# Kernel optimization log

Measured on AMD Instinct MI355X. Metric: run time of the kernel, lower is better.

## Reference

```python
import jax, jax.numpy as jnp
import numpy as np

N_NODES = 100000
N_EDGES = 3200000
IN_DIM = 64
N_SEQ = 8
HID1 = 256
HID2 = 128
END = 64
OUT = 1


def _glorot(key, shape):
    fan_in, fan_out = shape
    lim = (6.0 / (fan_in + fan_out)) ** 0.5
    return jax.random.uniform(key, shape, jnp.float32, -lim, lim)


def setup_inputs() -> dict:
    key = jax.random.key(0)
    ks = jax.random.split(key, 10)
    features = jax.random.normal(ks[0], (N_NODES, IN_DIM, N_SEQ), jnp.float32)
    src = jax.random.randint(ks[1], (N_EDGES,), 0, N_NODES, jnp.int32)
    dst = jax.random.randint(ks[2], (N_EDGES,), 0, N_NODES, jnp.int32)
    return {
        "features": features,
        "src": src,
        "dst": dst,
        "W1": _glorot(ks[3], (IN_DIM * N_SEQ, HID1)),
        "b1": jnp.zeros((HID1,), jnp.float32),
        "W2": _glorot(ks[4], (HID1, HID2)),
        "b2": jnp.zeros((HID2,), jnp.float32),
        "Wo1": _glorot(ks[5], (HID2, END)),
        "bo1": jnp.zeros((END,), jnp.float32),
        "Wo2": _glorot(ks[6], (END, OUT)),
        "bo2": jnp.zeros((OUT,), jnp.float32),
    }


def _graph_conv(x, src, dst, W, b):
    # DGL GraphConv, norm='both': D_out^{-1/2} pre-scale, sum-aggregate, D_in^{-1/2} post-scale.
    n = x.shape[0]
    ones = jnp.ones((src.shape[0],), x.dtype)
    deg_out = jnp.clip(jax.ops.segment_sum(ones, src, num_segments=n), 1.0)
    deg_in = jnp.clip(jax.ops.segment_sum(ones, dst, num_segments=n), 1.0)
    x = x * jax.lax.rsqrt(deg_out)[:, None]
    # mult-first vs aggregate-first is mathematically identical; project to smaller dim first
    if W.shape[0] > W.shape[1]:
        x = x @ W
        agg = jax.ops.segment_sum(x[src], dst, num_segments=n)
    else:
        agg = jax.ops.segment_sum(x[src], dst, num_segments=n) @ W
    return agg * jax.lax.rsqrt(deg_in)[:, None] + b


def reference(features, src, dst, W1, b1, W2, b2, Wo1, bo1, Wo2, bo2):
    x = features.reshape(features.shape[0], IN_DIM * N_SEQ)  # [N, in_dim*n_seq]
    x = jax.nn.relu(_graph_conv(x, src, dst, W1, b1))
    x = _graph_conv(x, src, dst, W2, b2)
    x = jax.nn.relu(x @ Wo1 + bo1)
    return x @ Wo2 + bo2
```

## Files before the change

### kernel.cpp

```cpp
#include <hip/hip_runtime.h>
#include <hip/hip_bf16.h>
#include <hip/hip_fp16.h>

#define N_NODES 100000
#define N_EDGES 3200000
#define DIM0 512
#define DIM1 256
#define DIM2 128
#define DIM3 64
#define NSB 98

#define HPART 16384
#define HPAIR 8192
#define NP 7
#define NSL 32
#define SLC (N_EDGES / NSL)

typedef _Float16 f16x8 __attribute__((ext_vector_type(8)));
typedef float f32x4 __attribute__((ext_vector_type(4)));


__global__ __launch_bounds__(256) void k_hist_priv(const int* __restrict__ src,
                                                   const int* __restrict__ dst,
                                                   unsigned* __restrict__ hp) {
    __shared__ unsigned h32[HPAIR];
    int blk = blockIdx.x, part = blockIdx.y, arr = blockIdx.z;
    const int* __restrict__ keys = arr ? dst : src;
    int base = part * HPART;
    for (int i = threadIdx.x; i < HPAIR; i += 256) h32[i] = 0;
    __syncthreads();
    int e0 = blk * SLC, e1 = e0 + SLC;
    for (int e = e0 + threadIdx.x; e < e1; e += 256) {
        int k = keys[e] - base;
        if ((unsigned)k < (unsigned)HPART)
            atomicAdd(&h32[k >> 1], 1u << ((k & 1) * 16));
    }
    __syncthreads();
    unsigned* out = hp + ((size_t)(arr * NP + part) * NSL + blk) * HPAIR;
    for (int i = threadIdx.x; i < HPAIR; i += 256) out[i] = h32[i];
}

__global__ __launch_bounds__(256) void k_reduce(unsigned* __restrict__ hp,
                                                int* __restrict__ cnt_out,
                                                int* __restrict__ cnt_in) {
    int idx = blockIdx.x * 256 + threadIdx.x;
    if (idx >= 2 * NP * HPAIR) return;
    int arr = idx / (NP * HPAIR);
    int rem = idx % (NP * HPAIR);
    int part = rem / HPAIR;
    int j = rem % HPAIR;
    unsigned* p = hp + ((size_t)(arr * NP + part) * NSL) * HPAIR + j;
    unsigned lo = 0, hi = 0;
    #pragma unroll 8
    for (int b = 0; b < NSL; ++b) {
        unsigned v = p[(size_t)b * HPAIR];
        if (arr == 1) p[(size_t)b * HPAIR] = (lo & 0xffffu) | (hi << 16);
        lo += v & 0xffffu;
        hi += v >> 16;
    }
    int node0 = part * HPART + 2 * j;
    int* cnt = arr ? cnt_in : cnt_out;
    if (node0 < N_NODES) cnt[node0] = (int)lo;
    if (node0 + 1 < N_NODES) cnt[node0 + 1] = (int)hi;
}

__global__ __launch_bounds__(1024) void k_scan_a(const int* __restrict__ cnt,
                                                 int* __restrict__ excl,
                                                 int* __restrict__ bsum) {
    __shared__ int buf[1024];
    int tid = threadIdx.x;
    int i = blockIdx.x * 1024 + tid;
    int v = (i < N_NODES) ? cnt[i] : 0;
    buf[tid] = v;
    __syncthreads();
    #pragma unroll
    for (int off = 1; off < 1024; off <<= 1) {
        int t = (tid >= off) ? buf[tid - off] : 0;
        __syncthreads();
        buf[tid] += t;
        __syncthreads();
    }
    if (i < N_NODES) excl[i] = buf[tid] - v;
    if (tid == 1023) bsum[blockIdx.x] = buf[1023];
}

__global__ __launch_bounds__(128) void k_scan_b(const int* __restrict__ bsum,
                                                int* __restrict__ boff) {
    __shared__ int buf[128];
    int tid = threadIdx.x;
    int v = (tid < NSB) ? bsum[tid] : 0;
    buf[tid] = v;
    __syncthreads();
    #pragma unroll
    for (int off = 1; off < 128; off <<= 1) {
        int t = (tid >= off) ? buf[tid - off] : 0;
        __syncthreads();
        buf[tid] += t;
        __syncthreads();
    }
    if (tid < NSB) boff[tid] = buf[tid] - v;
    if (tid == 127) boff[NSB] = buf[127];
}

__global__ __launch_bounds__(256) void k_scan_c(const int* __restrict__ excl,
                                                const int* __restrict__ boff,
                                                const int* __restrict__ cnt_out,
                                                const int* __restrict__ cnt_in,
                                                int* __restrict__ row_ptr,
                                                float* __restrict__ s_out,
                                                float* __restrict__ s_in) {
    int i = blockIdx.x * 256 + threadIdx.x;
    if (i < N_NODES) {
        row_ptr[i] = excl[i] + boff[i >> 10];
        int co = cnt_out[i]; if (co < 1) co = 1;
        int ci = cnt_in[i];  if (ci < 1) ci = 1;
        s_out[i] = rsqrtf((float)co);
        s_in[i]  = rsqrtf((float)ci);
    }
    if (i == 0) row_ptr[N_NODES] = boff[NSB];
}

__global__ __launch_bounds__(256) void k_scatter_nr(const int* __restrict__ src,
                                                    const int* __restrict__ dst,
                                                    const int* __restrict__ row_ptr,
                                                    const unsigned* __restrict__ hp,
                                                    int* __restrict__ esrc) {
    __shared__ int base_s[HPART];
    int blk = blockIdx.x, part = blockIdx.y;
    int pbase = part * HPART;
    const unsigned* off_p = hp + ((size_t)(1 * NP + part) * NSL + blk) * HPAIR;
    for (int k = threadIdx.x; k < HPART; k += 256) {
        int node = pbase + k;
        int rp = (node < N_NODES) ? row_ptr[node] : 0;
        unsigned w = off_p[k >> 1];
        unsigned off = (k & 1) ? (w >> 16) : (w & 0xffffu);
        base_s[k] = rp + (int)off;
    }
    __syncthreads();
    int e0 = blk * SLC, e1 = e0 + SLC;
    for (int e = e0 + threadIdx.x; e < e1; e += 256) {
        int d = dst[e];
        int k = d - pbase;
        if ((unsigned)k < (unsigned)HPART) {
            int p = atomicAdd(&base_s[k], 1);
            esrc[p] = src[e];
        }
    }
}


__global__ __launch_bounds__(256) void k_cvtW1(const float* __restrict__ W1,
                                               __half* __restrict__ W1t) {
    int idx = blockIdx.x * 256 + threadIdx.x;
    if (idx < DIM0 * DIM1) {
        int k = idx / DIM1, n = idx % DIM1;
        W1t[n * DIM0 + k] = __float2half(W1[idx]);
    }
}

__global__ __launch_bounds__(256) void k_cvtW2(const float* __restrict__ W2,
                                               __half* __restrict__ W2t) {
    int idx = blockIdx.x * 256 + threadIdx.x;
    if (idx < DIM1 * DIM2) {
        int k = idx / DIM2, n = idx % DIM2;
        W2t[n * DIM1 + k] = __float2half(W2[idx]);
    }
}


__global__ __launch_bounds__(256) void k_gemm1(const float* __restrict__ feat,
                                               const float* __restrict__ s_out,
                                               const __half* __restrict__ W1t,
                                               __half* __restrict__ y) {
    __shared__ __align__(16) _Float16 As[64][40];
    __shared__ __align__(16) _Float16 Bs[256][40];
    int tid = threadIdx.x;
    int wv = tid >> 6, lane = tid & 63;
    int m16 = lane & 15, quad = lane >> 4;
    int n0 = blockIdx.x * 64;

    int srow = tid >> 2;
    int scol = (tid & 3) * 8;
    int gr = n0 + srow;
    bool avalid = gr < N_NODES;
    int grc = avalid ? gr : (N_NODES - 1);
    float ascale = avalid ? s_out[gr] : 0.0f;
    const float* aptr = feat + (size_t)grc * DIM0 + scol;
    int bn = tid >> 2;
    int bc = (tid & 3) * 8;

    f32x4 acc[4][4] = {};
    for (int k0 = 0; k0 < DIM0; k0 += 32) {
        float4 f0 = *(const float4*)(aptr + k0);
        float4 f1 = *(const float4*)(aptr + k0 + 4);
        __syncthreads();
        {
            f16x8 h;
            h[0] = (_Float16)(f0.x * ascale); h[1] = (_Float16)(f0.y * ascale);
            h[2] = (_Float16)(f0.z * ascale); h[3] = (_Float16)(f0.w * ascale);
            h[4] = (_Float16)(f1.x * ascale); h[5] = (_Float16)(f1.y * ascale);
            h[6] = (_Float16)(f1.z * ascale); h[7] = (_Float16)(f1.w * ascale);
            *(f16x8*)&As[srow][scol] = h;
        }
        #pragma unroll
        for (int p = 0; p < 4; ++p) {
            int n = p * 64 + bn;
            f16x8 v = *(const f16x8*)(W1t + (size_t)n * DIM0 + k0 + bc);
            *(f16x8*)&Bs[n][bc] = v;
        }
        __syncthreads();
        f16x8 af[4], bf[4];
        #pragma unroll
        for (int r = 0; r < 4; ++r) af[r] = *(const f16x8*)&As[r * 16 + m16][quad * 8];
        #pragma unroll
        for (int c = 0; c < 4; ++c) bf[c] = *(const f16x8*)&Bs[wv * 64 + c * 16 + m16][quad * 8];
        #pragma unroll
        for (int r = 0; r < 4; ++r)
            #pragma unroll
            for (int c = 0; c < 4; ++c)
                acc[r][c] = __builtin_amdgcn_mfma_f32_16x16x32_f16(af[r], bf[c], acc[r][c], 0, 0, 0);
    }
    #pragma unroll
    for (int r = 0; r < 4; ++r) {
        #pragma unroll
        for (int i = 0; i < 4; ++i) {
            int row = n0 + r * 16 + quad * 4 + i;
            if (row < N_NODES) {
                #pragma unroll
                for (int c = 0; c < 4; ++c) {
                    int col = wv * 64 + c * 16 + m16;
                    y[(size_t)row * DIM1 + col] = __float2half(acc[r][c][i]);
                }
            }
        }
    }
}


__global__ __launch_bounds__(256) void k_agg256(const int* __restrict__ row_ptr,
                                                const int* __restrict__ esrc,
                                                const __half* __restrict__ y1,
                                                const float* __restrict__ s_in,
                                                const float* __restrict__ s_out,
                                                const float* __restrict__ b1,
                                                __half* __restrict__ x2) {
    int wave = threadIdx.x >> 6;
    int lane = threadIdx.x & 63;
    int n = blockIdx.x * 4 + wave;
    int beg = row_ptr[n], end = row_ptr[n + 1];
    const uint2* ybase = (const uint2*)y1;
    float4 acc = make_float4(0.f, 0.f, 0.f, 0.f);
    int i = beg;
    for (; i + 4 <= end; i += 4) {
        int s0 = esrc[i], s1 = esrc[i + 1], s2 = esrc[i + 2], s3 = esrc[i + 3];
        uint2 r0 = ybase[(size_t)s0 * 64 + lane];
        uint2 r1 = ybase[(size_t)s1 * 64 + lane];
        uint2 r2 = ybase[(size_t)s2 * 64 + lane];
        uint2 r3 = ybase[(size_t)s3 * 64 + lane];
        float2 a0 = __half22float2(*(__half2*)&r0.x), b0 = __half22float2(*(__half2*)&r0.y);
        float2 a1 = __half22float2(*(__half2*)&r1.x), b1v = __half22float2(*(__half2*)&r1.y);
        float2 a2 = __half22float2(*(__half2*)&r2.x), b2v = __half22float2(*(__half2*)&r2.y);
        float2 a3 = __half22float2(*(__half2*)&r3.x), b3v = __half22float2(*(__half2*)&r3.y);
        acc.x += a0.x + a1.x + a2.x + a3.x;
        acc.y += a0.y + a1.y + a2.y + a3.y;
        acc.z += b0.x + b1v.x + b2v.x + b3v.x;
        acc.w += b0.y + b1v.y + b2v.y + b3v.y;
    }
    for (; i < end; ++i) {
        uint2 r = ybase[(size_t)esrc[i] * 64 + lane];
        float2 a = __half22float2(*(__half2*)&r.x), b = __half22float2(*(__half2*)&r.y);
        acc.x += a.x; acc.y += a.y; acc.z += b.x; acc.w += b.y;
    }
    float si = s_in[n];
    float so = s_out[n];
    float4 bb = *(const float4*)&b1[lane * 4];
    acc.x = fmaxf(acc.x * si + bb.x, 0.f) * so;
    acc.y = fmaxf(acc.y * si + bb.y, 0.f) * so;
    acc.z = fmaxf(acc.z * si + bb.z, 0.f) * so;
    acc.w = fmaxf(acc.w * si + bb.w, 0.f) * so;
    union { uint2 u; __half2 h[2]; } cv;
    cv.h[0] = __floats2half2_rn(acc.x, acc.y);
    cv.h[1] = __floats2half2_rn(acc.z, acc.w);
    *(uint2*)&x2[(size_t)n * DIM1 + lane * 4] = cv.u;
}


__global__ __launch_bounds__(256) void k_gemm2(const __half* __restrict__ x2,
                                               const __half* __restrict__ W2t,
                                               __half* __restrict__ y) {
    __shared__ __align__(16) _Float16 As[64][40];
    __shared__ __align__(16) _Float16 Bs[128][40];
    int tid = threadIdx.x;
    int wv = tid >> 6, lane = tid & 63;
    int m16 = lane & 15, quad = lane >> 4;
    int n0 = blockIdx.x * 64;

    int srow = tid >> 2;
    int scol = (tid & 3) * 8;
    int gr = n0 + srow;
    int grc = (gr < N_NODES) ? gr : (N_NODES - 1);
    const __half* aptr = x2 + (size_t)grc * DIM1 + scol;
    int bn = tid >> 2;
    int bc = (tid & 3) * 8;

    f32x4 acc[4][2] = {};
    for (int k0 = 0; k0 < DIM1; k0 += 32) {
        f16x8 av = *(const f16x8*)(aptr + k0);
        __syncthreads();
        *(f16x8*)&As[srow][scol] = av;
        #pragma unroll
        for (int p = 0; p < 2; ++p) {
            int n = p * 64 + bn;
            f16x8 v = *(const f16x8*)(W2t + (size_t)n * DIM1 + k0 + bc);
            *(f16x8*)&Bs[n][bc] = v;
        }
        __syncthreads();
        f16x8 af[4], bf[2];
        #pragma unroll
        for (int r = 0; r < 4; ++r) af[r] = *(const f16x8*)&As[r * 16 + m16][quad * 8];
        #pragma unroll
        for (int c = 0; c < 2; ++c) bf[c] = *(const f16x8*)&Bs[wv * 32 + c * 16 + m16][quad * 8];
        #pragma unroll
        for (int r = 0; r < 4; ++r)
            #pragma unroll
            for (int c = 0; c < 2; ++c)
                acc[r][c] = __builtin_amdgcn_mfma_f32_16x16x32_f16(af[r], bf[c], acc[r][c], 0, 0, 0);
    }
    #pragma unroll
    for (int r = 0; r < 4; ++r) {
        #pragma unroll
        for (int i = 0; i < 4; ++i) {
            int row = n0 + r * 16 + quad * 4 + i;
            if (row < N_NODES) {
                #pragma unroll
                for (int c = 0; c < 2; ++c) {
                    int col = wv * 32 + c * 16 + m16;
                    y[(size_t)row * DIM2 + col] = __float2half(acc[r][c][i]);
                }
            }
        }
    }
}


__global__ __launch_bounds__(256) void k_agg_head(const int* __restrict__ row_ptr,
                                                  const int* __restrict__ esrc,
                                                  const __half* __restrict__ y2,
                                                  const float* __restrict__ s_in,
                                                  const float* __restrict__ b2,
                                                  const float* __restrict__ Wo1,
                                                  const float* __restrict__ bo1,
                                                  const float* __restrict__ Wo2,
                                                  const float* __restrict__ bo2,
                                                  float* __restrict__ out) {
    __shared__ __half2 w1p[DIM2 / 2][DIM3];
    __shared__ float w2s[DIM3];
    __shared__ float hs[4][DIM2];
    int tid = threadIdx.x;
    for (int i = tid; i < (DIM2 / 2) * DIM3; i += 256) {
        int m = i >> 6, l = i & 63;
        w1p[m][l] = __floats2half2_rn(Wo1[(2 * m) * DIM3 + l], Wo1[(2 * m + 1) * DIM3 + l]);
    }
    if (tid < DIM3) w2s[tid] = Wo2[tid];
    __syncthreads();

    int wave = tid >> 6, lane = tid & 63;
    int n = blockIdx.x * 4 + wave;
    int beg = row_ptr[n], end = row_ptr[n + 1];
    const unsigned* ybase = (const unsigned*)y2;
    float2 acc = make_float2(0.f, 0.f);
    int i = beg;
    for (; i + 4 <= end; i += 4) {
        unsigned r0 = ybase[(size_t)esrc[i] * 64 + lane];
        unsigned r1 = ybase[(size_t)esrc[i + 1] * 64 + lane];
        unsigned r2 = ybase[(size_t)esrc[i + 2] * 64 + lane];
        unsigned r3 = ybase[(size_t)esrc[i + 3] * 64 + lane];
        float2 f0 = __half22float2(*(__half2*)&r0);
        float2 f1 = __half22float2(*(__half2*)&r1);
        float2 f2 = __half22float2(*(__half2*)&r2);
        float2 f3 = __half22float2(*(__half2*)&r3);
        acc.x += f0.x + f1.x + f2.x + f3.x;
        acc.y += f0.y + f1.y + f2.y + f3.y;
    }
    for (; i < end; ++i) {
        unsigned r = ybase[(size_t)esrc[i] * 64 + lane];
        float2 f = __half22float2(*(__half2*)&r);
        acc.x += f.x; acc.y += f.y;
    }
    float si = s_in[n];
    float2 bv = *(const float2*)&b2[lane * 2];
    hs[wave][lane * 2 + 0] = acc.x * si + bv.x;
    hs[wave][lane * 2 + 1] = acc.y * si + bv.y;
    __syncthreads();

    float t = bo1[lane];
    #pragma unroll 8
    for (int m = 0; m < DIM2 / 2; ++m) {
        float2 h2 = *(const float2*)&hs[wave][2 * m];
        float2 wf = __half22float2(w1p[m][lane]);
        t += h2.x * wf.x + h2.y * wf.y;
    }
    t = fmaxf(t, 0.f);
    float p = t * w2s[lane];
    #pragma unroll
    for (int off = 32; off > 0; off >>= 1) p += __shfl_down(p, off);
    if (lane == 0) out[n] = p + bo2[0];
}


extern "C" void kernel_launch(void* const* d_in, const int* in_sizes, int n_in,
                              void* d_out, int out_size, void* d_ws, size_t ws_size,
                              hipStream_t stream) {
    const float* feat = (const float*)d_in[0];
    const int*   src  = (const int*)d_in[1];
    const int*   dst  = (const int*)d_in[2];
    const float* W1   = (const float*)d_in[3];
    const float* b1   = (const float*)d_in[4];
    const float* W2   = (const float*)d_in[5];
    const float* b2   = (const float*)d_in[6];
    const float* Wo1  = (const float*)d_in[7];
    const float* bo1  = (const float*)d_in[8];
    const float* Wo2  = (const float*)d_in[9];
    const float* bo2  = (const float*)d_in[10];
    float* out = (float*)d_out;

    char* ws = (char*)d_ws;
    size_t off = 0;
    auto alloc = [&](size_t bytes) -> char* {
        char* p = ws + off;
        off = (off + bytes + 255) & ~(size_t)255;
        return p;
    };
    int*      cnt_out = (int*)alloc(N_NODES * 4);
    int*      cnt_in  = (int*)alloc(N_NODES * 4);
    int*      row_ptr = (int*)alloc((N_NODES + 1) * 4);
    int*      excl    = (int*)alloc(N_NODES * 4);
    int*      bsum    = (int*)alloc((NSB + 1) * 4);
    int*      boff    = (int*)alloc((NSB + 1) * 4);
    int*      esrc    = (int*)alloc((size_t)N_EDGES * 4);
    unsigned* histp   = (unsigned*)alloc((size_t)2 * NP * NSL * HPAIR * 4);
    float*    s_out   = (float*)alloc(N_NODES * 4);
    float*    s_in    = (float*)alloc(N_NODES * 4);
    __half*   W1t     = (__half*)alloc((size_t)DIM0 * DIM1 * 2);
    __half*   W2t     = (__half*)alloc((size_t)DIM1 * DIM2 * 2);
    __half*   y1h     = (__half*)alloc((size_t)N_NODES * DIM1 * 2);
    __half*   x2h     = (__half*)alloc((size_t)N_NODES * DIM1 * 2);
    __half*   y2h     = (__half*)alloc((size_t)N_NODES * DIM2 * 2);

    k_hist_priv<<<dim3(NSL, NP, 2), 256, 0, stream>>>(src, dst, histp);
    k_reduce<<<(2 * NP * HPAIR + 255) / 256, 256, 0, stream>>>(histp, cnt_out, cnt_in);
    k_scan_a<<<NSB, 1024, 0, stream>>>(cnt_in, excl, bsum);
    k_scan_b<<<1, 128, 0, stream>>>(bsum, boff);
    k_scan_c<<<(N_NODES + 255) / 256, 256, 0, stream>>>(excl, boff, cnt_out, cnt_in,
                                                        row_ptr, s_out, s_in);
    k_scatter_nr<<<dim3(NSL, NP), 256, 0, stream>>>(src, dst, row_ptr, histp, esrc);

    k_cvtW1<<<(DIM0 * DIM1 + 255) / 256, 256, 0, stream>>>(W1, W1t);
    k_cvtW2<<<(DIM1 * DIM2 + 255) / 256, 256, 0, stream>>>(W2, W2t);

    int nblk = (N_NODES + 63) / 64;
    k_gemm1<<<nblk, 256, 0, stream>>>(feat, s_out, W1t, y1h);
    k_agg256<<<N_NODES / 4, 256, 0, stream>>>(row_ptr, esrc, y1h, s_in, s_out, b1, x2h);
    k_gemm2<<<nblk, 256, 0, stream>>>(x2h, W2t, y2h);
    k_agg_head<<<N_NODES / 4, 256, 0, stream>>>(row_ptr, esrc, y2h, s_in, b2,
                                                Wo1, bo1, Wo2, bo2, out);
}
```

Before: 1.166 ms.

## Widen aggregation gathers to 16B loads and split head into MFMA kernel

Both aggregation kernels now gather each neighbor row with 16-byte loads per lane. A wave processes 2 or 4 edges at once in subgroups and combines the partial sums with cross-lane shuffles. The fused aggregate+MLP head is split into a pure aggregation kernel that writes an fp16 intermediate, plus a separate MFMA-based head kernel that uses a pre-transposed fp16 Wo1. The goal is more bytes in flight per gather and removing the per-block shared-memory weight staging and scalar dot loop in the head. The cost is an extra intermediate buffer, an extra launch, and fp16 rounding of the head input.

```diff
diff --git a/kernel.cpp b/kernel.cpp
--- a/kernel.cpp
+++ b/kernel.cpp
@@ -149,21 +149,24 @@
 }
 
 
-__global__ __launch_bounds__(256) void k_cvtW1(const float* __restrict__ W1,
-                                               __half* __restrict__ W1t) {
+__global__ __launch_bounds__(256) void k_cvtW(const float* __restrict__ W1,
+                                              const float* __restrict__ W2,
+                                              const float* __restrict__ Wo1,
+                                              __half* __restrict__ W1t,
+                                              __half* __restrict__ W2t,
+                                              __half* __restrict__ Wo1t) {
     int idx = blockIdx.x * 256 + threadIdx.x;
     if (idx < DIM0 * DIM1) {
         int k = idx / DIM1, n = idx % DIM1;
         W1t[n * DIM0 + k] = __float2half(W1[idx]);
-    }
-}
-
-__global__ __launch_bounds__(256) void k_cvtW2(const float* __restrict__ W2,
-                                               __half* __restrict__ W2t) {
-    int idx = blockIdx.x * 256 + threadIdx.x;
-    if (idx < DIM1 * DIM2) {
-        int k = idx / DIM2, n = idx % DIM2;
-        W2t[n * DIM1 + k] = __float2half(W2[idx]);
+    } else if (idx < DIM0 * DIM1 + DIM1 * DIM2) {
+        int j = idx - DIM0 * DIM1;
+        int k = j / DIM2, n = j % DIM2;
+        W2t[n * DIM1 + k] = __float2half(W2[j]);
+    } else if (idx < DIM0 * DIM1 + DIM1 * DIM2 + DIM2 * DIM3) {
+        int j = idx - DIM0 * DIM1 - DIM1 * DIM2;
+        int k = j / DIM3, n = j % DIM3;
+        Wo1t[n * DIM2 + k] = __float2half(Wo1[j]);
     }
 }
 
@@ -246,42 +249,54 @@
                                                 __half* __restrict__ x2) {
     int wave = threadIdx.x >> 6;
     int lane = threadIdx.x & 63;
+    int sg = lane >> 5, cl = lane & 31;
     int n = blockIdx.x * 4 + wave;
     int beg = row_ptr[n], end = row_ptr[n + 1];
-    const uint2* ybase = (const uint2*)y1;
-    float4 acc = make_float4(0.f, 0.f, 0.f, 0.f);
-    int i = beg;
-    for (; i + 4 <= end; i += 4) {
-        int s0 = esrc[i], s1 = esrc[i + 1], s2 = esrc[i + 2], s3 = esrc[i + 3];
-        uint2 r0 = ybase[(size_t)s0 * 64 + lane];
-        uint2 r1 = ybase[(size_t)s1 * 64 + lane];
-        uint2 r2 = ybase[(size_t)s2 * 64 + lane];
-        uint2 r3 = ybase[(size_t)s3 * 64 + lane];
-        float2 a0 = __half22float2(*(__half2*)&r0.x), b0 = __half22float2(*(__half2*)&r0.y);
-        float2 a1 = __half22float2(*(__half2*)&r1.x), b1v = __half22float2(*(__half2*)&r1.y);
-        float2 a2 = __half22float2(*(__half2*)&r2.x), b2v = __half22float2(*(__half2*)&r2.y);
-        float2 a3 = __half22float2(*(__half2*)&r3.x), b3v = __half22float2(*(__half2*)&r3.y);
-        acc.x += a0.x + a1.x + a2.x + a3.x;
-        acc.y += a0.y + a1.y + a2.y + a3.y;
-        acc.z += b0.x + b1v.x + b2v.x + b3v.x;
-        acc.w += b0.y + b1v.y + b2v.y + b3v.y;
-    }
-    for (; i < end; ++i) {
-        uint2 r = ybase[(size_t)esrc[i] * 64 + lane];
-        float2 a = __half22float2(*(__half2*)&r.x), b = __half22float2(*(__half2*)&r.y);
-        acc.x += a.x; acc.y += a.y; acc.z += b.x; acc.w += b.y;
-    }
-    float si = s_in[n];
-    float so = s_out[n];
-    float4 bb = *(const float4*)&b1[lane * 4];
-    acc.x = fmaxf(acc.x * si + bb.x, 0.f) * so;
-    acc.y = fmaxf(acc.y * si + bb.y, 0.f) * so;
-    acc.z = fmaxf(acc.z * si + bb.z, 0.f) * so;
-    acc.w = fmaxf(acc.w * si + bb.w, 0.f) * so;
-    union { uint2 u; __half2 h[2]; } cv;
-    cv.h[0] = __floats2half2_rn(acc.x, acc.y);
-    cv.h[1] = __floats2half2_rn(acc.z, acc.w);
-    *(uint2*)&x2[(size_t)n * DIM1 + lane * 4] = cv.u;
+    const uint4* yb = (const uint4*)y1;
+    float acc[8] = {};
+    int cnt = end - beg;
+    int end2 = end - (cnt & 1);
+    for (int i = beg; i < end2; i += 2) {
+        int idx = esrc[i + sg];
+        uint4 v = yb[(size_t)idx * 32 + cl];
+        const __half2* hh = (const __half2*)&v;
+        #pragma unroll
+        for (int j = 0; j < 4; ++j) {
+            float2 f = __half22float2(hh[j]);
+            acc[2 * j] += f.x; acc[2 * j + 1] += f.y;
+        }
+    }
+    if ((cnt & 1) && sg == 0) {
+        int idx = esrc[end2];
+        uint4 v = yb[(size_t)idx * 32 + cl];
+        const __half2* hh = (const __half2*)&v;
+        #pragma unroll
+        for (int j = 0; j < 4; ++j) {
+            float2 f = __half22float2(hh[j]);
+            acc[2 * j] += f.x; acc[2 * j + 1] += f.y;
+        }
+    }
+    #pragma unroll
+    for (int j = 0; j < 8; ++j) acc[j] += __shfl_xor(acc[j], 32);
+    if (sg == 0) {
+        float si = s_in[n], so = s_out[n];
+        float4 ba = *(const float4*)&b1[cl * 8];
+        float4 bb = *(const float4*)&b1[cl * 8 + 4];
+        float r0 = fmaxf(acc[0] * si + ba.x, 0.f) * so;
+        float r1 = fmaxf(acc[1] * si + ba.y, 0.f) * so;
+        float r2 = fmaxf(acc[2] * si + ba.z, 0.f) * so;
+        float r3 = fmaxf(acc[3] * si + ba.w, 0.f) * so;
+        float r4 = fmaxf(acc[4] * si + bb.x, 0.f) * so;
+        float r5 = fmaxf(acc[5] * si + bb.y, 0.f) * so;
+        float r6 = fmaxf(acc[6] * si + bb.z, 0.f) * so;
+        float r7 = fmaxf(acc[7] * si + bb.w, 0.f) * so;
+        union { uint4 u; __half2 h[4]; } cv;
+        cv.h[0] = __floats2half2_rn(r0, r1);
+        cv.h[1] = __floats2half2_rn(r2, r3);
+        cv.h[2] = __floats2half2_rn(r4, r5);
+        cv.h[3] = __floats2half2_rn(r6, r7);
+        ((uint4*)x2)[(size_t)n * 32 + cl] = cv.u;
+    }
 }
 
 
@@ -343,68 +358,111 @@
 }
 
 
-__global__ __launch_bounds__(256) void k_agg_head(const int* __restrict__ row_ptr,
-                                                  const int* __restrict__ esrc,
-                                                  const __half* __restrict__ y2,
-                                                  const float* __restrict__ s_in,
-                                                  const float* __restrict__ b2,
-                                                  const float* __restrict__ Wo1,
-                                                  const float* __restrict__ bo1,
-                                                  const float* __restrict__ Wo2,
-                                                  const float* __restrict__ bo2,
-                                                  float* __restrict__ out) {
-    __shared__ __half2 w1p[DIM2 / 2][DIM3];
-    __shared__ float w2s[DIM3];
-    __shared__ float hs[4][DIM2];
-    int tid = threadIdx.x;
-    for (int i = tid; i < (DIM2 / 2) * DIM3; i += 256) {
-        int m = i >> 6, l = i & 63;
-        w1p[m][l] = __floats2half2_rn(Wo1[(2 * m) * DIM3 + l], Wo1[(2 * m + 1) * DIM3 + l]);
-    }
-    if (tid < DIM3) w2s[tid] = Wo2[tid];
-    __syncthreads();
-
-    int wave = tid >> 6, lane = tid & 63;
+__global__ __launch_bounds__(256) void k_agg128s(const int* __restrict__ row_ptr,
+                                                 const int* __restrict__ esrc,
+                                                 const __half* __restrict__ y2,
+                                                 const float* __restrict__ s_in,
+                                                 const float* __restrict__ b2,
+                                                 __half* __restrict__ xh) {
+    int wave = threadIdx.x >> 6;
+    int lane = threadIdx.x & 63;
+    int sg = lane >> 4, cl = lane & 15;
     int n = blockIdx.x * 4 + wave;
     int beg = row_ptr[n], end = row_ptr[n + 1];
-    const unsigned* ybase = (const unsigned*)y2;
-    float2 acc = make_float2(0.f, 0.f);
-    int i = beg;
-    for (; i + 4 <= end; i += 4) {
-        unsigned r0 = ybase[(size_t)esrc[i] * 64 + lane];
-        unsigned r1 = ybase[(size_t)esrc[i + 1] * 64 + lane];
-        unsigned r2 = ybase[(size_t)esrc[i + 2] * 64 + lane];
-        unsigned r3 = ybase[(size_t)esrc[i + 3] * 64 + lane];
-        float2 f0 = __half22float2(*(__half2*)&r0);
-        float2 f1 = __half22float2(*(__half2*)&r1);
-        float2 f2 = __half22float2(*(__half2*)&r2);
-        float2 f3 = __half22float2(*(__half2*)&r3);
-        acc.x += f0.x + f1.x + f2.x + f3.x;
-        acc.y += f0.y + f1.y + f2.y + f3.y;
-    }
-    for (; i < end; ++i) {
-        unsigned r = ybase[(size_t)esrc[i] * 64 + lane];
-        float2 f = __half22float2(*(__half2*)&r);
-        acc.x += f.x; acc.y += f.y;
-    }
-    float si = s_in[n];
-    float2 bv = *(const float2*)&b2[lane * 2];
-    hs[wave][lane * 2 + 0] = acc.x * si + bv.x;
-    hs[wave][lane * 2 + 1] = acc.y * si + bv.y;
-    __syncthreads();
-
-    float t = bo1[lane];
-    #pragma unroll 8
-    for (int m = 0; m < DIM2 / 2; ++m) {
-        float2 h2 = *(const float2*)&hs[wave][2 * m];
-        float2 wf = __half22float2(w1p[m][lane]);
-        t += h2.x * wf.x + h2.y * wf.y;
-    }
-    t = fmaxf(t, 0.f);
-    float p = t * w2s[lane];
-    #pragma unroll
-    for (int off = 32; off > 0; off >>= 1) p += __shfl_down(p, off);
-    if (lane == 0) out[n] = p + bo2[0];
+    const uint4* yb = (const uint4*)y2;
+    float acc[8] = {};
+    int cnt = end - beg;
+    int end4 = end - (cnt & 3);
+    for (int i = beg; i < end4; i += 4) {
+        int idx = esrc[i + sg];
+        uint4 v = yb[(size_t)idx * 16 + cl];
+        const __half2* hh = (const __half2*)&v;
+        #pragma unroll
+        for (int j = 0; j < 4; ++j) {
+            float2 f = __half22float2(hh[j]);
+            acc[2 * j] += f.x; acc[2 * j + 1] += f.y;
+        }
+    }
+    int rem = cnt & 3;
+    if (sg < rem) {
+        int idx = esrc[end4 + sg];
+        uint4 v = yb[(size_t)idx * 16 + cl];
+        const __half2* hh = (const __half2*)&v;
+        #pragma unroll
+        for (int j = 0; j < 4; ++j) {
+            float2 f = __half22float2(hh[j]);
+            acc[2 * j] += f.x; acc[2 * j + 1] += f.y;
+        }
+    }
+    #pragma unroll
+    for (int j = 0; j < 8; ++j) {
+        acc[j] += __shfl_xor(acc[j], 16);
+        acc[j] += __shfl_xor(acc[j], 32);
+    }
+    if (lane < 16) {
+        float si = s_in[n];
+        float4 ba = *(const float4*)&b2[cl * 8];
+        float4 bb = *(const float4*)&b2[cl * 8 + 4];
+        union { uint4 u; __half2 h[4]; } cv;
+        cv.h[0] = __floats2half2_rn(acc[0] * si + ba.x, acc[1] * si + ba.y);
+        cv.h[1] = __floats2half2_rn(acc[2] * si + ba.z, acc[3] * si + ba.w);
+        cv.h[2] = __floats2half2_rn(acc[4] * si + bb.x, acc[5] * si + bb.y);
+        cv.h[3] = __floats2half2_rn(acc[6] * si + bb.z, acc[7] * si + bb.w);
+        ((uint4*)xh)[(size_t)n * 16 + cl] = cv.u;
+    }
+}
+
+
+__global__ __launch_bounds__(256) void k_head(const __half* __restrict__ xh,
+                                              const __half* __restrict__ Wo1t,
+                                              const float* __restrict__ bo1,
+                                              const float* __restrict__ Wo2,
+                                              const float* __restrict__ bo2,
+                                              float* __restrict__ out) {
+    int tid = threadIdx.x;
+    int wv = tid >> 6, lane = tid & 63;
+    int m16 = lane & 15, quad = lane >> 4;
+    int n0 = (blockIdx.x * 4 + wv) * 16;
+    if (n0 >= N_NODES) return;
+    const uint4* A = (const uint4*)xh;
+    const uint4* B = (const uint4*)Wo1t;
+    f32x4 acc[4] = {};
+    #pragma unroll
+    for (int ks = 0; ks < 4; ++ks) {
+        uint4 av = A[(size_t)(n0 + m16) * 16 + ks * 4 + quad];
+        f16x8 af = *(const f16x8*)&av;
+        #pragma unroll
+        for (int ct = 0; ct < 4; ++ct) {
+            uint4 bv = B[(size_t)(ct * 16 + m16) * 16 + ks * 4 + quad];
+            f16x8 bf = *(const f16x8*)&bv;
+            acc[ct] = __builtin_amdgcn_mfma_f32_16x16x32_f16(af, bf, acc[ct], 0, 0, 0);
+        }
+    }
+    float bo1v[4], wo2v[4];
+    #pragma unroll
+    for (int ct = 0; ct < 4; ++ct) {
+        int col = ct * 16 + m16;
+        bo1v[ct] = bo1[col];
+        wo2v[ct] = Wo2[col];
+    }
+    float s[4];
+    #pragma unroll
+    for (int r = 0; r < 4; ++r) {
+        float t = 0.f;
+        #pragma unroll
+        for (int ct = 0; ct < 4; ++ct)
+            t += fmaxf(acc[ct][r] + bo1v[ct], 0.f) * wo2v[ct];
+        s[r] = t;
+    }
+    #pragma unroll
+    for (int off = 1; off <= 8; off <<= 1)
+        #pragma unroll
+        for (int r = 0; r < 4; ++r) s[r] += __shfl_xor(s[r], off);
+    if (m16 == 0) {
+        float bb = bo2[0];
+        #pragma unroll
+        for (int r = 0; r < 4; ++r) out[n0 + quad * 4 + r] = s[r] + bb;
+    }
 }
 
 
@@ -443,9 +501,11 @@
     float*    s_in    = (float*)alloc(N_NODES * 4);
     __half*   W1t     = (__half*)alloc((size_t)DIM0 * DIM1 * 2);
     __half*   W2t     = (__half*)alloc((size_t)DIM1 * DIM2 * 2);
+    __half*   Wo1t    = (__half*)alloc((size_t)DIM2 * DIM3 * 2);
     __half*   y1h     = (__half*)alloc((size_t)N_NODES * DIM1 * 2);
     __half*   x2h     = (__half*)alloc((size_t)N_NODES * DIM1 * 2);
     __half*   y2h     = (__half*)alloc((size_t)N_NODES * DIM2 * 2);
+    __half*   xhh     = (__half*)alloc((size_t)N_NODES * DIM2 * 2);
 
     k_hist_priv<<<dim3(NSL, NP, 2), 256, 0, stream>>>(src, dst, histp);
     k_reduce<<<(2 * NP * HPAIR + 255) / 256, 256, 0, stream>>>(histp, cnt_out, cnt_in);
@@ -455,13 +515,13 @@
                                                         row_ptr, s_out, s_in);
     k_scatter_nr<<<dim3(NSL, NP), 256, 0, stream>>>(src, dst, row_ptr, histp, esrc);
 
-    k_cvtW1<<<(DIM0 * DIM1 + 255) / 256, 256, 0, stream>>>(W1, W1t);
-    k_cvtW2<<<(DIM1 * DIM2 + 255) / 256, 256, 0, stream>>>(W2, W2t);
+    int cvt_total = DIM0 * DIM1 + DIM1 * DIM2 + DIM2 * DIM3;
+    k_cvtW<<<(cvt_total + 255) / 256, 256, 0, stream>>>(W1, W2, Wo1, W1t, W2t, Wo1t);
 
     int nblk = (N_NODES + 63) / 64;
     k_gemm1<<<nblk, 256, 0, stream>>>(feat, s_out, W1t, y1h);
     k_agg256<<<N_NODES / 4, 256, 0, stream>>>(row_ptr, esrc, y1h, s_in, s_out, b1, x2h);
     k_gemm2<<<nblk, 256, 0, stream>>>(x2h, W2t, y2h);
-    k_agg_head<<<N_NODES / 4, 256, 0, stream>>>(row_ptr, esrc, y2h, s_in, b2,
-                                                Wo1, bo1, Wo2, bo2, out);
-}
+    k_agg128s<<<N_NODES / 4, 256, 0, stream>>>(row_ptr, esrc, y2h, s_in, b2, xhh);
+    k_head<<<(N_NODES / 16 + 3) / 4, 256, 0, stream>>>(xhh, Wo1t, bo1, Wo2, bo2, out);
+}
```

Measured after the change: 1.101 ms. -5.6%, faster.
